# Performance work log

Hardware: AMD Instinct MI355X
Metric: run time of the kernel (lower is better)

## Reference

```python
import jax, jax.numpy as jnp
import numpy as np

B, S, D_IN, H, L = 32, 1024, 128, 256, 2
ND = 2  # bidirectional


def setup_inputs() -> dict:
    key = jax.random.key(0)
    ks = iter(jax.random.split(key, 40))

    def p(shape, scale=0.05):
        return jax.random.normal(next(ks), shape, dtype=jnp.float32) * scale

    inp = {"x": jax.random.normal(next(ks), (B, S, D_IN), dtype=jnp.float32)}
    dims_in = [D_IN, H * ND]
    for l in range(L):
        for tag in ("f", "b"):
            inp[f"w_ih_l{l}{tag}"] = p((4 * H, dims_in[l]))
            inp[f"w_hh_l{l}{tag}"] = p((4 * H, H))
            inp[f"b_l{l}{tag}"] = p((4 * H,))  # b_ih + b_hh fused (identical math)
    inp["attn_w"] = p((H * ND,))   # nn.Linear(2H, 1) weight
    inp["attn_b"] = p((1,))
    inp["head_w"] = p((D_IN, H * ND))  # forecasting head: Linear(2H, input_dim)
    inp["head_b"] = p((D_IN,))
    return inp


def _lstm_dir(x, w_ih, w_hh, b, reverse):
    """Single-direction LSTM over [B,S,F] -> [B,S,H]. PyTorch gate order i,f,g,o."""
    Bb = x.shape[0]
    Hh = w_hh.shape[1]
    # Precompute input projections once: [S,B,4H]
    xp = jnp.einsum('bsi,gi->sbg', x, w_ih) + b
    if reverse:
        xp = xp[::-1]
    h0 = jnp.zeros((Bb, Hh), x.dtype)
    c0 = jnp.zeros((Bb, Hh), x.dtype)

    def step(carry, gx):
        h, c = carry
        g = gx + h @ w_hh.T
        i, f, gg, o = jnp.split(g, 4, axis=-1)
        c = jax.nn.sigmoid(f) * c + jax.nn.sigmoid(i) * jnp.tanh(gg)
        h = jax.nn.sigmoid(o) * jnp.tanh(c)
        return (h, c), h

    _, hs = jax.lax.scan(step, (h0, c0), xp)
    if reverse:
        hs = hs[::-1]
    return jnp.swapaxes(hs, 0, 1)  # [B,S,H]


def reference(x,
              w_ih_l0f, w_hh_l0f, b_l0f, w_ih_l0b, w_hh_l0b, b_l0b,
              w_ih_l1f, w_hh_l1f, b_l1f, w_ih_l1b, w_hh_l1b, b_l1b,
              attn_w, attn_b, head_w, head_b):
    h = x
    layers = [((w_ih_l0f, w_hh_l0f, b_l0f), (w_ih_l0b, w_hh_l0b, b_l0b)),
              ((w_ih_l1f, w_hh_l1f, b_l1f), (w_ih_l1b, w_hh_l1b, b_l1b))]
    for fw, bw in layers:
        hf = _lstm_dir(h, *fw, False)
        hb = _lstm_dir(h, *bw, True)
        h = jnp.concatenate([hf, hb], axis=-1)  # [B,S,2H]; dropout off (eval)
    # Prefix attention pooling: original recomputes softmax over output[:, :i+1]
    # for every i. Equivalently (softmax is shift-invariant per prefix):
    # context_i = cumsum(e * h)_i / cumsum(e)_i with e = exp(s - max(s)).
    s = h @ attn_w + attn_b[0]                      # [B,S] attention scores
    e = jnp.exp(s - jnp.max(s, axis=1, keepdims=True))
    num = jnp.cumsum(e[..., None] * h, axis=1)      # [B,S,2H]
    den = jnp.cumsum(e, axis=1)[..., None]          # [B,S,1]
    context = num / den                             # [B,S,2H]
    forecasts = context @ head_w.T + head_b         # [B,S,D_IN]
    return forecasts
```

## Files before the change

### kernel.cpp

```cpp
#include <hip/hip_runtime.h>

typedef unsigned short ushort_t;
typedef unsigned int uint_t;
typedef unsigned long long u64;
typedef __attribute__((ext_vector_type(8))) short short8;
typedef __attribute__((ext_vector_type(4))) float floatx4;

#define S_LEN 1024
#define BATCH 32
#define HDIM  256
#define GDIM  1024
#define DIN   128

__device__ __forceinline__ float bf2f(ushort_t u) { return __uint_as_float(((unsigned)u) << 16); }
__device__ __forceinline__ float bf2fs(short s)   { return __uint_as_float(((unsigned)(unsigned short)s) << 16); }
__device__ __forceinline__ ushort_t f2bf(float f) {
  unsigned u = __float_as_uint(f);
  unsigned r = (u + 0x7fffu + ((u >> 16) & 1u)) >> 16;
  return (ushort_t)r;
}
__device__ __forceinline__ float sigf(float x) { return 1.f / (1.f + __expf(-x)); }
__device__ __forceinline__ float tanh_f(float x) {
  float ax = fabsf(x);
  float e = __expf(2.f * ax);
  float r = 1.f - 2.f / (e + 1.f);
  return x < 0.f ? -r : r;
}

__device__ __forceinline__ void load_lds16(const void* g, void* l) {
  __builtin_amdgcn_global_load_lds((const __attribute__((address_space(1))) unsigned int*)g,
                                   (__attribute__((address_space(3))) unsigned int*)l, 16, 0, 0);
}
__device__ __forceinline__ void vm0() { asm volatile("s_waitcnt vmcnt(0)" ::: "memory"); }

__device__ __forceinline__ void lds_barrier() {
  __builtin_amdgcn_sched_barrier(0);
  asm volatile("s_waitcnt lgkmcnt(0)" ::: "memory");
  __builtin_amdgcn_s_barrier();
  __builtin_amdgcn_sched_barrier(0);
}

__global__ __launch_bounds__(256) void gemm_bf16(
    const ushort_t* __restrict__ A, const ushort_t* __restrict__ Bw,
    const float* __restrict__ bias, void* __restrict__ Cout,
    int M, int N, int K, int mode)
{
  __shared__ __align__(16) ushort_t As[128 * 64];
  __shared__ __align__(16) ushort_t Bs[128 * 64];
  const int tid = threadIdx.x;
  const int lane = tid & 63, wid = tid >> 6;
  const int wm = wid >> 1, wn = wid & 1;
  const int bm = blockIdx.y, bn = blockIdx.x;
  const int l15 = lane & 15, q4 = lane >> 4;

  const int r  = tid >> 3;
  const int c8 = tid & 7;
  const int g8 = c8 ^ (r & 7);

  floatx4 zero4 = {0.f, 0.f, 0.f, 0.f};
  floatx4 acc[4][4];
#pragma unroll
  for (int mt = 0; mt < 4; ++mt)
#pragma unroll
    for (int nt = 0; nt < 4; ++nt) acc[mt][nt] = zero4;

  for (int k0 = 0; k0 < K; k0 += 64) {
    __syncthreads();
#pragma unroll
    for (int p = 0; p < 4; ++p) {
      int row = p * 32 + r;
      load_lds16(A + (size_t)(bm * 128 + row) * K + k0 + g8 * 8, (void*)(As + p * 2048 + wid * 512));
      load_lds16(Bw + (size_t)(bn * 128 + row) * K + k0 + g8 * 8, (void*)(Bs + p * 2048 + wid * 512));
    }
    __syncthreads();
#pragma unroll
    for (int ks = 0; ks < 2; ++ks) {
      const int kk = ks * 4 + q4;
      short8 af[4], bf[4];
#pragma unroll
      for (int mt = 0; mt < 4; ++mt) {
        int row = wm * 64 + mt * 16 + l15;
        af[mt] = *(const short8*)(As + row * 64 + ((kk ^ (row & 7)) << 3));
      }
#pragma unroll
      for (int nt = 0; nt < 4; ++nt) {
        int row = wn * 64 + nt * 16 + l15;
        bf[nt] = *(const short8*)(Bs + row * 64 + ((kk ^ (row & 7)) << 3));
      }
#pragma unroll
      for (int mt = 0; mt < 4; ++mt)
#pragma unroll
        for (int nt = 0; nt < 4; ++nt)
          acc[mt][nt] = __builtin_amdgcn_mfma_f32_16x16x32_bf16(af[mt], bf[nt], acc[mt][nt], 0, 0, 0);
    }
  }

#pragma unroll
  for (int mt = 0; mt < 4; ++mt)
#pragma unroll
    for (int nt = 0; nt < 4; ++nt)
#pragma unroll
      for (int rr = 0; rr < 4; ++rr) {
        int m = bm * 128 + wm * 64 + mt * 16 + q4 * 4 + rr;
        int n = bn * 128 + wn * 64 + nt * 16 + l15;
        float v = acc[mt][nt][rr] + bias[n];
        if (mode == 0) {
          ((ushort_t*)Cout)[(size_t)m * N + n] = f2bf(v);
        } else if (mode == 1) {
          int t = m >> 5, b = m & 31;
          ((float*)Cout)[(size_t)b * (S_LEN * DIN) + t * DIN + n] = v;
        } else {
          int t = m >> 5, b = m & 31;
          ((ushort_t*)Cout)[(size_t)t * (N * 32) + n * 32 + b] = f2bf(v);
        }
      }
}

__global__ __launch_bounds__(256) void lstm_layer(
    const ushort_t* __restrict__ xpf, const ushort_t* __restrict__ xpb,
    const ushort_t* __restrict__ whhf, const ushort_t* __restrict__ whhb,
    ushort_t* __restrict__ hout, u64* __restrict__ comm, u64* __restrict__ epochs)
{
  const int bx = blockIdx.x;
  const int dir = bx & 1, j = bx >> 1;

  const ushort_t* xp  = dir ? xpb : xpf;
  const ushort_t* whh = dir ? whhb : whhf;
  u64* commd = comm + (size_t)dir * 4096;
  const int hoff = dir * 256;

  __shared__ __align__(16) ushort_t hbuf[32 * 264];
  __shared__ __align__(16) float stage[32 * 133];

  const int tid = threadIdx.x, lane = tid & 63, w = tid >> 6;
  const int l15 = lane & 15, q4 = lane >> 4;

  short8 Bf[2][8];
#pragma unroll
  for (int tl = 0; tl < 2; ++tl) {
    int grow = w * 256 + j * 32 + tl * 16 + l15;
#pragma unroll
    for (int ks = 0; ks < 8; ++ks)
      Bf[tl][ks] = *(const short8*)(whh + (size_t)grow * 256 + ks * 32 + q4 * 8);
  }

  for (int i = tid; i < 32 * 132; i += 256) ((uint_t*)hbuf)[i] = 0u;

  float cst[4] = {0.f, 0.f, 0.f, 0.f};

  u64 xr64[2][2];
  auto ldxp = [&](int tt) {
#pragma unroll
    for (int mt = 0; mt < 2; ++mt)
#pragma unroll
      for (int tl = 0; tl < 2; ++tl) {
        int g = w * 256 + j * 32 + tl * 16 + l15;
        xr64[mt][tl] = *(const u64*)(xp + (size_t)tt * (GDIM * BATCH) + (size_t)g * 32 + mt * 16 + q4 * 4);
      }
  };

  const int cb  = tid >> 3;
  const int cg0 = tid & 7;
  const int c4  = (tid & 7) * 4;

  ldxp((dir == 0) ? 0 : 1023);
  __syncthreads();

  for (int sc = 0; sc < 1024; ++sc) {
    const int tcur  = (dir == 0) ? sc : 1023 - sc;
    const int tnext = (dir == 0) ? (sc < 1023 ? sc + 1 : 1023) : (sc < 1023 ? 1022 - sc : 0);

    floatx4 acc[2][2];
#pragma unroll
    for (int mt = 0; mt < 2; ++mt)
#pragma unroll
      for (int tl = 0; tl < 2; ++tl) {
        u64 v = xr64[mt][tl];
#pragma unroll
        for (int rr = 0; rr < 4; ++rr)
          acc[mt][tl][rr] = bf2f((ushort_t)(v >> (16 * rr)));
      }

    ldxp(tnext);

    if (sc > 0) {
      const u64 want = (u64)(unsigned)sc;
      const u64* ea = epochs + ((size_t)(dir * 2 + (sc & 1)) * 8 + (lane & 7)) * 16;
      for (;;) {
        u64 v = (lane < 8) ? __hip_atomic_load(ea, __ATOMIC_RELAXED, __HIP_MEMORY_SCOPE_AGENT)
                           : want;
        if (__ballot(v >= want) == ~0ULL) break;
      }
      if (cg0 != j) {
        const u64* rbuf = commd + (size_t)(sc & 1) * 2048 + (size_t)cb * 64 + cg0 * 8;
        u64 tmp[8];
#pragma unroll
        for (int k = 0; k < 8; ++k)
          tmp[k] = __hip_atomic_load(rbuf + k, __ATOMIC_RELAXED, __HIP_MEMORY_SCOPE_AGENT);
#pragma unroll
        for (int k = 0; k < 8; ++k)
          *(u64*)(hbuf + cb * 264 + cg0 * 32 + k * 4) = tmp[k];
      }
    }
    lds_barrier();

#pragma unroll
    for (int ks = 0; ks < 8; ++ks) {
      short8 a0 = *(const short8*)(hbuf + l15 * 264 + ks * 32 + q4 * 8);
      short8 a1 = *(const short8*)(hbuf + (16 + l15) * 264 + ks * 32 + q4 * 8);
      acc[0][0] = __builtin_amdgcn_mfma_f32_16x16x32_bf16(a0, Bf[0][ks], acc[0][0], 0, 0, 0);
      acc[0][1] = __builtin_amdgcn_mfma_f32_16x16x32_bf16(a0, Bf[1][ks], acc[0][1], 0, 0, 0);
      acc[1][0] = __builtin_amdgcn_mfma_f32_16x16x32_bf16(a1, Bf[0][ks], acc[1][0], 0, 0, 0);
      acc[1][1] = __builtin_amdgcn_mfma_f32_16x16x32_bf16(a1, Bf[1][ks], acc[1][1], 0, 0, 0);
    }

#pragma unroll
    for (int mt = 0; mt < 2; ++mt)
#pragma unroll
      for (int tl = 0; tl < 2; ++tl)
#pragma unroll
        for (int rr = 0; rr < 4; ++rr)
          stage[(mt * 16 + q4 * 4 + rr) * 133 + w * 32 + tl * 16 + l15] = acc[mt][tl][rr];
    lds_barrier();

    float hv4[4];
#pragma unroll
    for (int i = 0; i < 4; ++i) {
      float gi = stage[cb * 133 +      c4 + i];
      float gf = stage[cb * 133 + 32 + c4 + i];
      float gg = stage[cb * 133 + 64 + c4 + i];
      float go = stage[cb * 133 + 96 + c4 + i];
      float c = sigf(gf) * cst[i] + sigf(gi) * tanh_f(gg);
      cst[i] = c;
      hv4[i] = sigf(go) * tanh_f(c);
    }
    u64 pv = (u64)f2bf(hv4[0]) | ((u64)f2bf(hv4[1]) << 16) |
             ((u64)f2bf(hv4[2]) << 32) | ((u64)f2bf(hv4[3]) << 48);

    __hip_atomic_store(commd + (size_t)((sc + 1) & 1) * 2048 + (size_t)cb * 64 + j * 8 + (tid & 7),
                       pv, __ATOMIC_RELAXED, __HIP_MEMORY_SCOPE_AGENT);
    *(u64*)(hbuf + cb * 264 + j * 32 + c4) = pv;
    vm0();
    __builtin_amdgcn_sched_barrier(0);
    __builtin_amdgcn_s_barrier();
    __builtin_amdgcn_sched_barrier(0);
    if (tid == 0)
      __hip_atomic_store(epochs + ((size_t)(dir * 2 + ((sc + 1) & 1)) * 8 + j) * 16,
                         (u64)(unsigned)(sc + 1), __ATOMIC_RELAXED, __HIP_MEMORY_SCOPE_AGENT);

    *(u64*)(hout + (size_t)tcur * (BATCH * 512) + cb * 512 + hoff + j * 32 + c4) = pv;
  }
}

__global__ __launch_bounds__(256) void attn_scores(
    const ushort_t* __restrict__ h1, const float* __restrict__ attn_w,
    const float* __restrict__ attn_b, float* __restrict__ e_out)
{
  const int b = blockIdx.x;
  __shared__ float sbuf[1024];
  __shared__ float red[4];
  const int tid = threadIdx.x, lane = tid & 63, w = tid >> 6;

  float wreg[8];
#pragma unroll
  for (int i = 0; i < 8; ++i) wreg[i] = attn_w[lane * 8 + i];

  for (int t = w; t < 1024; t += 4) {
    short8 hv = *(const short8*)(h1 + (size_t)t * (BATCH * 512) + b * 512 + lane * 8);
    float dot = 0.f;
#pragma unroll
    for (int i = 0; i < 8; ++i) dot += bf2fs(hv[i]) * wreg[i];
#pragma unroll
    for (int off = 32; off; off >>= 1) dot += __shfl_xor(dot, off);
    if (lane == 0) sbuf[t] = dot + attn_b[0];
  }
  __syncthreads();
  float m = -1e30f;
  for (int t = tid; t < 1024; t += 256) m = fmaxf(m, sbuf[t]);
#pragma unroll
  for (int off = 32; off; off >>= 1) m = fmaxf(m, __shfl_xor(m, off));
  if (lane == 0) red[w] = m;
  __syncthreads();
  float mm = fmaxf(fmaxf(red[0], red[1]), fmaxf(red[2], red[3]));
  for (int t = tid; t < 1024; t += 256) e_out[b * 1024 + t] = __expf(sbuf[t] - mm);
}

__global__ __launch_bounds__(256) void attn_ctx(
    const ushort_t* __restrict__ h1, const float* __restrict__ e_in, ushort_t* __restrict__ ctx)
{
  const int b = blockIdx.x >> 1, half = blockIdx.x & 1;
  const int c = half * 256 + threadIdx.x;
  float num = 0.f, den = 0.f;
  const ushort_t* hp = h1 + b * 512 + c;
  ushort_t* cp = ctx + b * 512 + c;
  const float* ep = e_in + b * 1024;
#pragma unroll 4
  for (int t = 0; t < 1024; ++t) {
    float ev = ep[t];
    float hv = bf2f(hp[(size_t)t * (BATCH * 512)]);
    num += ev * hv;
    den += ev;
    cp[(size_t)t * (BATCH * 512)] = f2bf(num / den);
  }
}

__global__ void castw(const float* __restrict__ in, ushort_t* __restrict__ out, int n) {
  int i = blockIdx.x * 256 + threadIdx.x;
  if (i < n) out[i] = f2bf(in[i]);
}
__global__ void castx(const float* __restrict__ x, ushort_t* __restrict__ xt) {
  int i = blockIdx.x * 256 + threadIdx.x;
  int dcol = i & 127;
  int m = i >> 7;
  int b = m & 31, s = m >> 5;
  xt[i] = f2bf(x[(size_t)b * (S_LEN * DIN) + s * DIN + dcol]);
}

extern "C" void kernel_launch(void* const* d_in, const int* in_sizes, int n_in,
                              void* d_out, int out_size, void* d_ws, size_t ws_size,
                              hipStream_t stream)
{
  const float* x     = (const float*)d_in[0];
  const float* wih0f = (const float*)d_in[1];
  const float* whh0f = (const float*)d_in[2];
  const float* b0f   = (const float*)d_in[3];
  const float* wih0b = (const float*)d_in[4];
  const float* whh0b = (const float*)d_in[5];
  const float* b0b   = (const float*)d_in[6];
  const float* wih1f = (const float*)d_in[7];
  const float* whh1f = (const float*)d_in[8];
  const float* b1f   = (const float*)d_in[9];
  const float* wih1b = (const float*)d_in[10];
  const float* whh1b = (const float*)d_in[11];
  const float* b1b   = (const float*)d_in[12];
  const float* attw  = (const float*)d_in[13];
  const float* attb  = (const float*)d_in[14];
  const float* headw = (const float*)d_in[15];
  const float* headb = (const float*)d_in[16];
  float* out = (float*)d_out;

  char* p = (char*)d_ws;
  auto alloc = [&](size_t bytes) {
    char* r = p;
    p += (bytes + 511) & ~(size_t)511;
    return r;
  };
  u64* ep0        = (u64*)alloc(512 * 8);
  u64* ep1        = (u64*)alloc(512 * 8);
  u64* comm0      = (u64*)alloc(8192 * 8);
  u64* comm1      = (u64*)alloc(8192 * 8);
  ushort_t* xt    = (ushort_t*)alloc((size_t)32768 * 128 * 2);
  ushort_t* cwih0f = (ushort_t*)alloc(131072 * 2);
  ushort_t* cwih0b = (ushort_t*)alloc(131072 * 2);
  ushort_t* cwhh0f = (ushort_t*)alloc(262144 * 2);
  ushort_t* cwhh0b = (ushort_t*)alloc(262144 * 2);
  ushort_t* cwih1f = (ushort_t*)alloc(524288 * 2);
  ushort_t* cwih1b = (ushort_t*)alloc(524288 * 2);
  ushort_t* cwhh1f = (ushort_t*)alloc(262144 * 2);
  ushort_t* cwhh1b = (ushort_t*)alloc(262144 * 2);
  ushort_t* cwhead = (ushort_t*)alloc(65536 * 2);
  ushort_t* xpA = (ushort_t*)alloc((size_t)32768 * 1024 * 2);
  ushort_t* xpB = (ushort_t*)alloc((size_t)32768 * 1024 * 2);
  ushort_t* h0  = (ushort_t*)alloc((size_t)32768 * 512 * 2);
  ushort_t* h1  = (ushort_t*)alloc((size_t)32768 * 512 * 2);
  float* ebuf   = (float*)alloc(32 * 1024 * 4);
  ushort_t* ctx = xpA;

  (void)in_sizes; (void)n_in; (void)out_size; (void)ws_size;

  (void)hipMemsetAsync(ep0, 0, 2 * 512 * 8, stream);

  castw<<<512, 256, 0, stream>>>(wih0f, cwih0f, 131072);
  castw<<<512, 256, 0, stream>>>(wih0b, cwih0b, 131072);
  castw<<<1024, 256, 0, stream>>>(whh0f, cwhh0f, 262144);
  castw<<<1024, 256, 0, stream>>>(whh0b, cwhh0b, 262144);
  castw<<<2048, 256, 0, stream>>>(wih1f, cwih1f, 524288);
  castw<<<2048, 256, 0, stream>>>(wih1b, cwih1b, 524288);
  castw<<<1024, 256, 0, stream>>>(whh1f, cwhh1f, 262144);
  castw<<<1024, 256, 0, stream>>>(whh1b, cwhh1b, 262144);
  castw<<<256, 256, 0, stream>>>(headw, cwhead, 65536);
  castx<<<16384, 256, 0, stream>>>(x, xt);

  gemm_bf16<<<dim3(8, 256), 256, 0, stream>>>(xt, cwih0f, b0f, xpA, 32768, 1024, 128, 2);
  gemm_bf16<<<dim3(8, 256), 256, 0, stream>>>(xt, cwih0b, b0b, xpB, 32768, 1024, 128, 2);
  lstm_layer<<<16, 256, 0, stream>>>(xpA, xpB, cwhh0f, cwhh0b, h0, comm0, ep0);

  gemm_bf16<<<dim3(8, 256), 256, 0, stream>>>(h0, cwih1f, b1f, xpA, 32768, 1024, 512, 2);
  gemm_bf16<<<dim3(8, 256), 256, 0, stream>>>(h0, cwih1b, b1b, xpB, 32768, 1024, 512, 2);
  lstm_layer<<<16, 256, 0, stream>>>(xpA, xpB, cwhh1f, cwhh1b, h1, comm1, ep1);

  attn_scores<<<32, 256, 0, stream>>>(h1, attw, attb, ebuf);
  attn_ctx<<<64, 256, 0, stream>>>(h1, ebuf, ctx);
  gemm_bf16<<<dim3(1, 256), 256, 0, stream>>>(ctx, cwhead, headb, out, 32768, 128, 512, 1);
}
```

Before: 7.595 ms.

## Split LSTM recurrence across two 512-thread blocks per direction with tagged-data exchange

The recurrent LSTM kernel now uses 2 blocks of 512 threads per direction instead of 8 blocks of 256. Each block owns 128 hidden units and holds all four gate rows for them in registers, so the gate nonlinearity is applied directly on the MFMA accumulators and the LDS staging pass goes away. Cross-block exchange drops the separate epoch flags: each bf16 value is packed with a 16-bit step tag, and readers spin until the tags match. This cuts the per-step barrier and handshake cost, but each block now does four times the MFMA work per step, and the tag scheme relies on 16-bit step numbers and 64-bit store atomicity.

```diff
diff --git a/kernel.cpp b/kernel.cpp
--- a/kernel.cpp
+++ b/kernel.cpp
@@ -5,6 +5,7 @@
 typedef unsigned long long u64;
 typedef __attribute__((ext_vector_type(8))) short short8;
 typedef __attribute__((ext_vector_type(4))) float floatx4;
+typedef __attribute__((ext_vector_type(4))) uint_t uintx4;
 
 #define S_LEN 1024
 #define BATCH 32
@@ -31,7 +32,6 @@
   __builtin_amdgcn_global_load_lds((const __attribute__((address_space(1))) unsigned int*)g,
                                    (__attribute__((address_space(3))) unsigned int*)l, 16, 0, 0);
 }
-__device__ __forceinline__ void vm0() { asm volatile("s_waitcnt vmcnt(0)" ::: "memory"); }
 
 __device__ __forceinline__ void lds_barrier() {
   __builtin_amdgcn_sched_barrier(0);
@@ -116,52 +116,57 @@
       }
 }
 
-__global__ __launch_bounds__(256) void lstm_layer(
+__global__ __launch_bounds__(512, 2) void lstm_layer(
     const ushort_t* __restrict__ xpf, const ushort_t* __restrict__ xpb,
     const ushort_t* __restrict__ whhf, const ushort_t* __restrict__ whhb,
-    ushort_t* __restrict__ hout, u64* __restrict__ comm, u64* __restrict__ epochs)
+    ushort_t* __restrict__ hout, uint_t* __restrict__ comm)
 {
   const int bx = blockIdx.x;
-  const int dir = bx & 1, j = bx >> 1;
+  const int dir = bx & 1, half = bx >> 1;
 
   const ushort_t* xp  = dir ? xpb : xpf;
   const ushort_t* whh = dir ? whhb : whhf;
-  u64* commd = comm + (size_t)dir * 4096;
+  uint_t* commd = comm + (size_t)dir * 16384;
   const int hoff = dir * 256;
+  const int choff = half * 128;
 
   __shared__ __align__(16) ushort_t hbuf[32 * 264];
-  __shared__ __align__(16) float stage[32 * 133];
 
   const int tid = threadIdx.x, lane = tid & 63, w = tid >> 6;
   const int l15 = lane & 15, q4 = lane >> 4;
 
-  short8 Bf[2][8];
-#pragma unroll
-  for (int tl = 0; tl < 2; ++tl) {
-    int grow = w * 256 + j * 32 + tl * 16 + l15;
+  short8 Bf[4][8];
+#pragma unroll
+  for (int gg = 0; gg < 4; ++gg) {
+    int grow = gg * 256 + choff + w * 16 + l15;
 #pragma unroll
     for (int ks = 0; ks < 8; ++ks)
-      Bf[tl][ks] = *(const short8*)(whh + (size_t)grow * 256 + ks * 32 + q4 * 8);
+      Bf[gg][ks] = *(const short8*)(whh + (size_t)grow * 256 + ks * 32 + q4 * 8);
   }
 
-  for (int i = tid; i < 32 * 132; i += 256) ((uint_t*)hbuf)[i] = 0u;
-
-  float cst[4] = {0.f, 0.f, 0.f, 0.f};
-
-  u64 xr64[2][2];
+  for (int i = tid; i < 32 * 132; i += 512) ((uint_t*)hbuf)[i] = 0u;
+
+  float cst[2][4];
+#pragma unroll
+  for (int mt = 0; mt < 2; ++mt)
+#pragma unroll
+    for (int rr = 0; rr < 4; ++rr) cst[mt][rr] = 0.f;
+
+  u64 xr64[4][2];
   auto ldxp = [&](int tt) {
 #pragma unroll
-    for (int mt = 0; mt < 2; ++mt)
-#pragma unroll
-      for (int tl = 0; tl < 2; ++tl) {
-        int g = w * 256 + j * 32 + tl * 16 + l15;
-        xr64[mt][tl] = *(const u64*)(xp + (size_t)tt * (GDIM * BATCH) + (size_t)g * 32 + mt * 16 + q4 * 4);
+    for (int gg = 0; gg < 4; ++gg)
+#pragma unroll
+      for (int mt = 0; mt < 2; ++mt) {
+        int g = gg * 256 + choff + w * 16 + l15;
+        xr64[gg][mt] = *(const u64*)(xp + (size_t)tt * (GDIM * BATCH) + (size_t)g * 32 + mt * 16 + q4 * 4);
       }
   };
 
-  const int cb  = tid >> 3;
-  const int cg0 = tid & 7;
-  const int c4  = (tid & 7) * 4;
+  const int cb2 = tid >> 4;
+  const int ch  = tid & 15;
+  const int obase = choff + ch * 8;
+  const int rbase = (128 - choff) + ch * 8;
 
   ldxp((dir == 0) ? 0 : 1023);
   __syncthreads();
@@ -170,37 +175,42 @@
     const int tcur  = (dir == 0) ? sc : 1023 - sc;
     const int tnext = (dir == 0) ? (sc < 1023 ? sc + 1 : 1023) : (sc < 1023 ? 1022 - sc : 0);
 
-    floatx4 acc[2][2];
-#pragma unroll
-    for (int mt = 0; mt < 2; ++mt)
-#pragma unroll
-      for (int tl = 0; tl < 2; ++tl) {
-        u64 v = xr64[mt][tl];
+    floatx4 acc[4][2];
+#pragma unroll
+    for (int gg = 0; gg < 4; ++gg)
+#pragma unroll
+      for (int mt = 0; mt < 2; ++mt) {
+        u64 v = xr64[gg][mt];
 #pragma unroll
         for (int rr = 0; rr < 4; ++rr)
-          acc[mt][tl][rr] = bf2f((ushort_t)(v >> (16 * rr)));
+          acc[gg][mt][rr] = bf2f((ushort_t)(v >> (16 * rr)));
       }
 
     ldxp(tnext);
 
     if (sc > 0) {
-      const u64 want = (u64)(unsigned)sc;
-      const u64* ea = epochs + ((size_t)(dir * 2 + (sc & 1)) * 8 + (lane & 7)) * 16;
-      for (;;) {
-        u64 v = (lane < 8) ? __hip_atomic_load(ea, __ATOMIC_RELAXED, __HIP_MEMORY_SCOPE_AGENT)
-                           : want;
-        if (__ballot(v >= want) == ~0ULL) break;
-      }
-      if (cg0 != j) {
-        const u64* rbuf = commd + (size_t)(sc & 1) * 2048 + (size_t)cb * 64 + cg0 * 8;
-        u64 tmp[8];
-#pragma unroll
-        for (int k = 0; k < 8; ++k)
-          tmp[k] = __hip_atomic_load(rbuf + k, __ATOMIC_RELAXED, __HIP_MEMORY_SCOPE_AGENT);
-#pragma unroll
-        for (int k = 0; k < 8; ++k)
-          *(u64*)(hbuf + cb * 264 + cg0 * 32 + k * 4) = tmp[k];
-      }
+      const uint_t want = (uint_t)sc;
+      const uint_t* rb = commd + (size_t)(sc & 1) * 8192 + cb2 * 256 + rbase;
+      while ((__hip_atomic_load(rb, __ATOMIC_RELAXED, __HIP_MEMORY_SCOPE_AGENT) & 0xffffu) != want) { }
+      const u64* rb64 = (const u64*)rb;
+      u64 wv[4];
+#pragma unroll
+      for (int k = 0; k < 4; ++k)
+        wv[k] = __hip_atomic_load(rb64 + k, __ATOMIC_RELAXED, __HIP_MEMORY_SCOPE_AGENT);
+#pragma unroll
+      for (int k = 0; k < 4; ++k) {
+        while ((((uint_t)wv[k] & 0xffffu) != want) | (((uint_t)(wv[k] >> 32) & 0xffffu) != want))
+          wv[k] = __hip_atomic_load(rb64 + k, __ATOMIC_RELAXED, __HIP_MEMORY_SCOPE_AGENT);
+      }
+      uint_t p[4];
+#pragma unroll
+      for (int k = 0; k < 4; ++k) {
+        uint_t c0 = (uint_t)(wv[k] >> 16) & 0xffffu;
+        uint_t c1 = (uint_t)(wv[k] >> 48);
+        p[k] = c0 | (c1 << 16);
+      }
+      *(u64*)(hbuf + cb2 * 264 + rbase)     = (u64)p[0] | ((u64)p[1] << 32);
+      *(u64*)(hbuf + cb2 * 264 + rbase + 4) = (u64)p[2] | ((u64)p[3] << 32);
     }
     lds_barrier();
 
@@ -208,47 +218,44 @@
     for (int ks = 0; ks < 8; ++ks) {
       short8 a0 = *(const short8*)(hbuf + l15 * 264 + ks * 32 + q4 * 8);
       short8 a1 = *(const short8*)(hbuf + (16 + l15) * 264 + ks * 32 + q4 * 8);
-      acc[0][0] = __builtin_amdgcn_mfma_f32_16x16x32_bf16(a0, Bf[0][ks], acc[0][0], 0, 0, 0);
-      acc[0][1] = __builtin_amdgcn_mfma_f32_16x16x32_bf16(a0, Bf[1][ks], acc[0][1], 0, 0, 0);
-      acc[1][0] = __builtin_amdgcn_mfma_f32_16x16x32_bf16(a1, Bf[0][ks], acc[1][0], 0, 0, 0);
-      acc[1][1] = __builtin_amdgcn_mfma_f32_16x16x32_bf16(a1, Bf[1][ks], acc[1][1], 0, 0, 0);
+#pragma unroll
+      for (int gg = 0; gg < 4; ++gg) {
+        acc[gg][0] = __builtin_amdgcn_mfma_f32_16x16x32_bf16(a0, Bf[gg][ks], acc[gg][0], 0, 0, 0);
+        acc[gg][1] = __builtin_amdgcn_mfma_f32_16x16x32_bf16(a1, Bf[gg][ks], acc[gg][1], 0, 0, 0);
+      }
     }
 
 #pragma unroll
     for (int mt = 0; mt < 2; ++mt)
 #pragma unroll
-      for (int tl = 0; tl < 2; ++tl)
-#pragma unroll
-        for (int rr = 0; rr < 4; ++rr)
-          stage[(mt * 16 + q4 * 4 + rr) * 133 + w * 32 + tl * 16 + l15] = acc[mt][tl][rr];
+      for (int rr = 0; rr < 4; ++rr) {
+        float gi = acc[0][mt][rr];
+        float gf = acc[1][mt][rr];
+        float gz = acc[2][mt][rr];
+        float go = acc[3][mt][rr];
+        float c = sigf(gf) * cst[mt][rr] + sigf(gi) * tanh_f(gz);
+        cst[mt][rr] = c;
+        float hv = sigf(go) * tanh_f(c);
+        hbuf[(mt * 16 + q4 * 4 + rr) * 264 + choff + w * 16 + l15] = f2bf(hv);
+      }
     lds_barrier();
 
-    float hv4[4];
-#pragma unroll
-    for (int i = 0; i < 4; ++i) {
-      float gi = stage[cb * 133 +      c4 + i];
-      float gf = stage[cb * 133 + 32 + c4 + i];
-      float gg = stage[cb * 133 + 64 + c4 + i];
-      float go = stage[cb * 133 + 96 + c4 + i];
-      float c = sigf(gf) * cst[i] + sigf(gi) * tanh_f(gg);
-      cst[i] = c;
-      hv4[i] = sigf(go) * tanh_f(c);
+    {
+      uintx4 hv = *(const uintx4*)(hbuf + cb2 * 264 + obase);
+      const uint_t tag = (uint_t)(sc + 1);
+      u64* cd = (u64*)(commd + (size_t)((sc + 1) & 1) * 8192 + cb2 * 256 + obase);
+      uint_t t0, t1;
+      t0 = ((hv.x & 0xffffu) << 16) | tag;  t1 = (hv.x & 0xffff0000u) | tag;
+      __hip_atomic_store(cd + 0, (u64)t0 | ((u64)t1 << 32), __ATOMIC_RELAXED, __HIP_MEMORY_SCOPE_AGENT);
+      t0 = ((hv.y & 0xffffu) << 16) | tag;  t1 = (hv.y & 0xffff0000u) | tag;
+      __hip_atomic_store(cd + 1, (u64)t0 | ((u64)t1 << 32), __ATOMIC_RELAXED, __HIP_MEMORY_SCOPE_AGENT);
+      t0 = ((hv.z & 0xffffu) << 16) | tag;  t1 = (hv.z & 0xffff0000u) | tag;
+      __hip_atomic_store(cd + 2, (u64)t0 | ((u64)t1 << 32), __ATOMIC_RELAXED, __HIP_MEMORY_SCOPE_AGENT);
+      t0 = ((hv.w & 0xffffu) << 16) | tag;  t1 = (hv.w & 0xffff0000u) | tag;
+      __hip_atomic_store(cd + 3, (u64)t0 | ((u64)t1 << 32), __ATOMIC_RELAXED, __HIP_MEMORY_SCOPE_AGENT);
+
+      *(uintx4*)(hout + (size_t)tcur * (BATCH * 512) + cb2 * 512 + hoff + obase) = hv;
     }
-    u64 pv = (u64)f2bf(hv4[0]) | ((u64)f2bf(hv4[1]) << 16) |
-             ((u64)f2bf(hv4[2]) << 32) | ((u64)f2bf(hv4[3]) << 48);
-
-    __hip_atomic_store(commd + (size_t)((sc + 1) & 1) * 2048 + (size_t)cb * 64 + j * 8 + (tid & 7),
-                       pv, __ATOMIC_RELAXED, __HIP_MEMORY_SCOPE_AGENT);
-    *(u64*)(hbuf + cb * 264 + j * 32 + c4) = pv;
-    vm0();
-    __builtin_amdgcn_sched_barrier(0);
-    __builtin_amdgcn_s_barrier();
-    __builtin_amdgcn_sched_barrier(0);
-    if (tid == 0)
-      __hip_atomic_store(epochs + ((size_t)(dir * 2 + ((sc + 1) & 1)) * 8 + j) * 16,
-                         (u64)(unsigned)(sc + 1), __ATOMIC_RELAXED, __HIP_MEMORY_SCOPE_AGENT);
-
-    *(u64*)(hout + (size_t)tcur * (BATCH * 512) + cb * 512 + hoff + j * 32 + c4) = pv;
   }
 }
 
@@ -345,10 +352,8 @@
     p += (bytes + 511) & ~(size_t)511;
     return r;
   };
-  u64* ep0        = (u64*)alloc(512 * 8);
-  u64* ep1        = (u64*)alloc(512 * 8);
-  u64* comm0      = (u64*)alloc(8192 * 8);
-  u64* comm1      = (u64*)alloc(8192 * 8);
+  uint_t* comm0   = (uint_t*)alloc(32768 * 4);
+  uint_t* comm1   = (uint_t*)alloc(32768 * 4);
   ushort_t* xt    = (ushort_t*)alloc((size_t)32768 * 128 * 2);
   ushort_t* cwih0f = (ushort_t*)alloc(131072 * 2);
   ushort_t* cwih0b = (ushort_t*)alloc(131072 * 2);
@@ -368,7 +373,7 @@
 
   (void)in_sizes; (void)n_in; (void)out_size; (void)ws_size;
 
-  (void)hipMemsetAsync(ep0, 0, 2 * 512 * 8, stream);
+  (void)hipMemsetAsync(comm0, 0, 2 * 32768 * 4, stream);
 
   castw<<<512, 256, 0, stream>>>(wih0f, cwih0f, 131072);
   castw<<<512, 256, 0, stream>>>(wih0b, cwih0b, 131072);
@@ -383,11 +388,11 @@
 
   gemm_bf16<<<dim3(8, 256), 256, 0, stream>>>(xt, cwih0f, b0f, xpA, 32768, 1024, 128, 2);
   gemm_bf16<<<dim3(8, 256), 256, 0, stream>>>(xt, cwih0b, b0b, xpB, 32768, 1024, 128, 2);
-  lstm_layer<<<16, 256, 0, stream>>>(xpA, xpB, cwhh0f, cwhh0b, h0, comm0, ep0);
+  lstm_layer<<<4, 512, 0, stream>>>(xpA, xpB, cwhh0f, cwhh0b, h0, comm0);
 
   gemm_bf16<<<dim3(8, 256), 256, 0, stream>>>(h0, cwih1f, b1f, xpA, 32768, 1024, 512, 2);
   gemm_bf16<<<dim3(8, 256), 256, 0, stream>>>(h0, cwih1b, b1b, xpB, 32768, 1024, 512, 2);
-  lstm_layer<<<16, 256, 0, stream>>>(xpA, xpB, cwhh1f, cwhh1b, h1, comm1, ep1);
+  lstm_layer<<<4, 512, 0, stream>>>(xpA, xpB, cwhh1f, cwhh1b, h1, comm1);
 
   attn_scores<<<32, 256, 0, stream>>>(h1, attw, attb, ebuf);
   attn_ctx<<<64, 256, 0, stream>>>(h1, ebuf, ctx);
```

New measurement: 13.54 ms. 1.78x slower.
